# Optimization experiments

Measured on AMD Instinct MI355X. Metric: run time of the kernel, lower is better.

The kernel has to match this reference:

```python
import jax, jax.numpy as jnp
import numpy as np

TEMPERATURE = 0.08
NEG = -9e15  # matches torch masked_fill value
EPS = 1e-8   # F.cosine_similarity eps


def setup_inputs() -> dict:
    key = jax.random.key(0)
    inputs = jax.random.normal(key, (8192, 512), dtype=jnp.float32)
    return {"inputs": inputs}


def reference(inputs):
    N = inputs.shape[0]
    # cosine similarity via normalize + GEMM (avoids NxNxD broadcast)
    norms = jnp.maximum(jnp.linalg.norm(inputs, axis=-1, keepdims=True), EPS)
    z = inputs / norms
    sim = z @ z.T  # [N, N]
    # mask self-similarity BEFORE temperature scaling (as in the torch code)
    diag = jnp.eye(N, dtype=bool)
    sim = jnp.where(diag, NEG, sim)
    sim = sim / TEMPERATURE
    # positive of row i is column (i - N//2) % N (eye rolled by N//2 along dim 0)
    idx = jnp.arange(N)
    pos_idx = (idx - N // 2) % N
    pos = jnp.take_along_axis(sim, pos_idx[:, None], axis=1)[:, 0]  # [N]
    nll = jnp.mean(-pos + jax.scipy.special.logsumexp(sim, axis=-1))
    # rank of the positive: counting-based equivalent of
    # cat([pos, sim_masked]).argsort(desc).argmin() with stable ties
    masked = sim.at[idx, pos_idx].set(NEG)
    positive_ranking = jnp.sum(masked > pos[:, None], axis=-1)  # [N] int
    return positive_ranking, nll
```

## Files before the change

### kernel.cpp

```cpp
#include <hip/hip_runtime.h>
#include <cstdint>
#include <cstddef>

#define NROW 8192
#define DIM  512
#define HALF 4096
#define INV_T 12.5f
#define LDSW 64

typedef __bf16 bf16x8  __attribute__((ext_vector_type(8)));
typedef float  floatx4 __attribute__((ext_vector_type(4)));

__device__ __forceinline__ float bf2f_lo(unsigned u) { return __uint_as_float(u << 16); }
__device__ __forceinline__ float bf2f_hi(unsigned u) { return __uint_as_float(u & 0xffff0000u); }
__device__ __forceinline__ unsigned short f2bf(float f) {
    unsigned u = __float_as_uint(f);
    u += 0x7fffu + ((u >> 16) & 1u);
    return (unsigned short)(u >> 16);
}

__device__ __forceinline__ void atom_addf(float* p, float v) {
    __hip_atomic_fetch_add(p, v, __ATOMIC_RELAXED, __HIP_MEMORY_SCOPE_AGENT);
}

__global__ void knormpos(const float* __restrict__ x, unsigned short* __restrict__ z,
                         float* __restrict__ pos, float* __restrict__ sumexp,
                         float* __restrict__ cnt, float* __restrict__ nll_acc,
                         int* __restrict__ done) {
    int id = blockIdx.x * 256 + threadIdx.x;
    if (id < NROW) { sumexp[id] = 0.f; cnt[id] = 0.f; }
    if (id == 0) { nll_acc[0] = 0.f; done[0] = 0; }

    __shared__ __align__(16) unsigned short zs[4][512];

    const int w = threadIdx.x >> 6, lane = threadIdx.x & 63;
    const int row = blockIdx.x * 2 + (w & 1) + (w >> 1) * HALF;

    const float* xr = x + (size_t)row * DIM + lane * 8;
    float4 v0 = ((const float4*)xr)[0];
    float4 v1 = ((const float4*)xr)[1];
    float ss = v0.x*v0.x + v0.y*v0.y + v0.z*v0.z + v0.w*v0.w
             + v1.x*v1.x + v1.y*v1.y + v1.z*v1.z + v1.w*v1.w;
    #pragma unroll
    for (int m = 1; m < 64; m <<= 1) ss += __shfl_xor(ss, m);
    float inv = 1.0f / fmaxf(sqrtf(ss), 1e-8f);
    uint4 o;
    o.x = (unsigned)f2bf(v0.x * inv) | ((unsigned)f2bf(v0.y * inv) << 16);
    o.y = (unsigned)f2bf(v0.z * inv) | ((unsigned)f2bf(v0.w * inv) << 16);
    o.z = (unsigned)f2bf(v1.x * inv) | ((unsigned)f2bf(v1.y * inv) << 16);
    o.w = (unsigned)f2bf(v1.z * inv) | ((unsigned)f2bf(v1.w * inv) << 16);
    *(uint4*)(&zs[w][lane * 8]) = o;
    int sl = (lane & 56) | ((lane & 7) ^ (row & 7));
    *(uint4*)(z + (size_t)row * DIM + sl * 8) = o;
    __syncthreads();

    if (w < 2) {
        uint4 a = *(const uint4*)(&zs[w][lane * 8]);
        uint4 b = *(const uint4*)(&zs[w + 2][lane * 8]);
        float s = bf2f_lo(a.x)*bf2f_lo(b.x) + bf2f_hi(a.x)*bf2f_hi(b.x)
                + bf2f_lo(a.y)*bf2f_lo(b.y) + bf2f_hi(a.y)*bf2f_hi(b.y)
                + bf2f_lo(a.z)*bf2f_lo(b.z) + bf2f_hi(a.z)*bf2f_hi(b.z)
                + bf2f_lo(a.w)*bf2f_lo(b.w) + bf2f_hi(a.w)*bf2f_hi(b.w);
        #pragma unroll
        for (int m = 1; m < 64; m <<= 1) s += __shfl_xor(s, m);
        if (lane == 0) {
            const int r = blockIdx.x * 2 + w;
            pos[r] = s;
            pos[r + HALF] = s;
        }
    }
}

__global__ __launch_bounds__(512, 3) void kgemm(const unsigned short* __restrict__ z,
                                                const float* __restrict__ pos,
                                                float* __restrict__ sumexp,
                                                float* __restrict__ cnt) {
    __shared__ __align__(16) unsigned short As[128 * LDSW];
    __shared__ __align__(16) unsigned short Bs[128 * LDSW];
    __shared__ float pos_r[128];
    __shared__ float pos_c[128];

    const int b = blockIdx.x;
    int I = 0;
    while (b >= 516 * (I + 1) - 32 * (I + 1) * (I + 1)) ++I;
    const int lb = b - (516 * I - 32 * I * I);
    int bi, bj;
    if (lb < 36) {
        int ti = 0;
        while (lb >= 8 * (ti + 1) - (ti + 1) * ti / 2) ++ti;
        const int tj = ti + (lb - (8 * ti - ti * (ti - 1) / 2));
        bi = I * 8 + ti;
        bj = I * 8 + tj;
    } else {
        const int o = lb - 36;
        const int J = I + 1 + (o >> 6);
        bi = I * 8 + ((o & 63) >> 3);
        bj = J * 8 + (o & 7);
    }
    const int r0 = bi * 128;
    const int c0 = bj * 128;
    const bool offdiag = (bi != bj);

    const int t = threadIdx.x;
    const int w = t >> 6, lane = t & 63;
    const int wm = w >> 1, wn = w & 1;
    const int cid = lane & 15, q = lane >> 4;

    if (t < 128) pos_r[t] = pos[r0 + t];
    else if (t < 256) pos_c[t - 128] = pos[c0 + (t - 128)];

    floatx4 acc[2][4];
    #pragma unroll
    for (int i = 0; i < 2; ++i)
        #pragma unroll
        for (int j = 0; j < 4; ++j)
            acc[i][j] = floatx4{0.f, 0.f, 0.f, 0.f};

    const int lrow8 = lane >> 3;
    const int lcol  = (lane & 7) * 8;

    for (int kk = 0; kk < 8; ++kk) {
        const int k0 = kk * 64;
        #pragma unroll
        for (int it = 0; it < 2; ++it) {
            const int c = it * 8 + w;
            const unsigned short* gA = z + (size_t)(r0 + c * 8 + lrow8) * DIM + k0 + lcol;
            const unsigned short* gB = z + (size_t)(c0 + c * 8 + lrow8) * DIM + k0 + lcol;
            __builtin_amdgcn_global_load_lds(
                (const __attribute__((address_space(1))) unsigned int*)gA,
                (__attribute__((address_space(3))) unsigned int*)(As + c * 512),
                16, 0, 0);
            __builtin_amdgcn_global_load_lds(
                (const __attribute__((address_space(1))) unsigned int*)gB,
                (__attribute__((address_space(3))) unsigned int*)(Bs + c * 512),
                16, 0, 0);
        }
        __syncthreads();
        #pragma unroll
        for (int ks = 0; ks < 2; ++ks) {
            bf16x8 af[2], bfv[4];
            #pragma unroll
            for (int f = 0; f < 2; ++f) {
                const int ar = wm * 32 + f * 16 + cid;
                const int pa = (4 * ks + q) ^ (ar & 7);
                af[f] = *(const bf16x8*)(As + ar * LDSW + pa * 8);
            }
            #pragma unroll
            for (int f = 0; f < 4; ++f) {
                const int br = wn * 64 + f * 16 + cid;
                const int pb = (4 * ks + q) ^ (br & 7);
                bfv[f] = *(const bf16x8*)(Bs + br * LDSW + pb * 8);
            }
            #pragma unroll
            for (int fm = 0; fm < 2; ++fm)
                #pragma unroll
                for (int fn = 0; fn < 4; ++fn)
                    acc[fm][fn] = __builtin_amdgcn_mfma_f32_16x16x32_bf16(
                        af[fm], bfv[fn], acc[fm][fn], 0, 0, 0);
        }
        __syncthreads();
    }

    float col_e[4] = {0.f, 0.f, 0.f, 0.f};
    float col_c[4] = {0.f, 0.f, 0.f, 0.f};
    #pragma unroll
    for (int fm = 0; fm < 2; ++fm) {
        #pragma unroll
        for (int r = 0; r < 4; ++r) {
            const int li = wm * 32 + fm * 16 + q * 4 + r;
            const int i  = r0 + li;
            const float pv = pos_r[li];
            const int pj = (i + HALF) & (NROW - 1);
            float es = 0.f, cs = 0.f;
            #pragma unroll
            for (int fn = 0; fn < 4; ++fn) {
                const int lj = wn * 64 + fn * 16 + cid;
                const int j  = c0 + lj;
                const float s = acc[fm][fn][r];
                const float e = __expf((s - 1.0f) * INV_T);
                const bool dg = (j == i);
                es += dg ? 0.f : e;
                cs += (!dg && (j != pj) && (s > pv)) ? 1.f : 0.f;
                col_e[fn] += e;
                const int pjc = (j + HALF) & (NROW - 1);
                col_c[fn] += ((i != pjc) && (s > pos_c[lj])) ? 1.f : 0.f;
            }
            #pragma unroll
            for (int m = 1; m < 16; m <<= 1) {
                es += __shfl_xor(es, m);
                cs += __shfl_xor(cs, m);
            }
            if (cid == 0) {
                atom_addf(&sumexp[i], es);
                atom_addf(&cnt[i], cs);
            }
        }
    }

    if (offdiag) {
        #pragma unroll
        for (int fn = 0; fn < 4; ++fn) {
            float ec = col_e[fn], cc = col_c[fn];
            ec += __shfl_xor(ec, 16); ec += __shfl_xor(ec, 32);
            cc += __shfl_xor(cc, 16); cc += __shfl_xor(cc, 32);
            if (q == 0) {
                const int j = c0 + wn * 64 + fn * 16 + cid;
                atom_addf(&sumexp[j], ec);
                atom_addf(&cnt[j], cc);
            }
        }
    }
}

__global__ void NCELoss_3126736191777_kernel(const float* __restrict__ cnt,
                                             const float* __restrict__ sumexp,
                                             const float* __restrict__ pos,
                                             float* __restrict__ out,
                                             float* __restrict__ nll_acc,
                                             int* __restrict__ done) {
    __shared__ float red[4];
    const int t = threadIdx.x;
    const int r = blockIdx.x * 256 + t;
    float c = cnt[r], se = sumexp[r], p = pos[r];
    float v;
    if (p != p || fabsf(p) > 1.05f) v = 60000.0f;
    else if (se == 0.0f)            v = 40000.0f;
    else if (c < 0.0f)              v = 25000.0f;
    else                            v = c;
    out[r] = v;
    float local = -p * INV_T + INV_T + __logf(se);
    #pragma unroll
    for (int m = 1; m < 64; m <<= 1) local += __shfl_xor(local, m);
    if ((t & 63) == 0) red[t >> 6] = local;
    __syncthreads();
    if (t == 0) {
        atom_addf(nll_acc, red[0] + red[1] + red[2] + red[3]);
        __threadfence();
        int ticket = __hip_atomic_fetch_add(done, 1, __ATOMIC_ACQ_REL,
                                            __HIP_MEMORY_SCOPE_AGENT);
        if (ticket == (int)gridDim.x - 1) {
            __threadfence();
            out[NROW] = nll_acc[0] / (float)NROW;
        }
    }
}

extern "C" void kernel_launch(void* const* d_in, const int* in_sizes, int n_in,
                              void* d_out, int out_size, void* d_ws, size_t ws_size,
                              hipStream_t stream) {
    (void)in_sizes; (void)n_in; (void)out_size; (void)ws_size;
    const float* x = (const float*)d_in[0];

    char* base = (char*)d_ws;
    float* pos     = (float*)(base);
    float* sumexp  = (float*)(base + (size_t)NROW * 4);
    float* cnt     = (float*)(base + (size_t)NROW * 8);
    float* nll_acc = (float*)(base + (size_t)NROW * 12);
    int*   done    = (int*)(base + (size_t)NROW * 12 + 64);
    unsigned short* z = (unsigned short*)(base + (size_t)NROW * 12 + 4096);
    float* out = (float*)d_out;

    knormpos<<<NROW / 4, 256, 0, stream>>>(x, z, pos, sumexp, cnt, nll_acc, done);
    kgemm<<<2080, 512, 0, stream>>>(z, pos, sumexp, cnt);
    NCELoss_3126736191777_kernel<<<NROW / 256, 256, 0, stream>>>(cnt, sumexp, pos, out, nll_acc, done);
}
```

Before: 166.0 us.

## Enlarge GEMM block tile to 128x256 over symmetric upper-triangle tiles

```diff
diff --git a/kernel.cpp b/kernel.cpp
--- a/kernel.cpp
+++ b/kernel.cpp
@@ -76,42 +76,34 @@
                                                 float* __restrict__ sumexp,
                                                 float* __restrict__ cnt) {
     __shared__ __align__(16) unsigned short As[128 * LDSW];
-    __shared__ __align__(16) unsigned short Bs[128 * LDSW];
+    __shared__ __align__(16) unsigned short Bs[256 * LDSW];
     __shared__ float pos_r[128];
-    __shared__ float pos_c[128];
-
-    const int b = blockIdx.x;
-    int I = 0;
-    while (b >= 516 * (I + 1) - 32 * (I + 1) * (I + 1)) ++I;
-    const int lb = b - (516 * I - 32 * I * I);
-    int bi, bj;
-    if (lb < 36) {
-        int ti = 0;
-        while (lb >= 8 * (ti + 1) - (ti + 1) * ti / 2) ++ti;
-        const int tj = ti + (lb - (8 * ti - ti * (ti - 1) / 2));
-        bi = I * 8 + ti;
-        bj = I * 8 + tj;
-    } else {
-        const int o = lb - 36;
-        const int J = I + 1 + (o >> 6);
-        bi = I * 8 + ((o & 63) >> 3);
-        bj = J * 8 + (o & 7);
-    }
+    __shared__ float pos_c[256];
+
+    int rem = blockIdx.x;
+    int bi = 0;
+    while (rem >= 32 - (bi >> 1)) { rem -= 32 - (bi >> 1); ++bi; }
+    const int J = (bi >> 1) + rem;
+    const bool hasB0 = (2 * J >= bi);
     const int r0 = bi * 128;
-    const int c0 = bj * 128;
-    const bool offdiag = (bi != bj);
+    const int c00 = J * 256;
 
     const int t = threadIdx.x;
     const int w = t >> 6, lane = t & 63;
-    const int wm = w >> 1, wn = w & 1;
+    const int wm = w >> 2, wn = w & 3;
     const int cid = lane & 15, q = lane >> 4;
 
+    const int Tl = wn >> 1;
+    const int bjw = 2 * J + Tl;
+    const bool valid = (Tl == 1) || hasB0;
+    const bool offd  = (bjw != bi);
+
     if (t < 128) pos_r[t] = pos[r0 + t];
-    else if (t < 256) pos_c[t - 128] = pos[c0 + (t - 128)];
-
-    floatx4 acc[2][4];
-    #pragma unroll
-    for (int i = 0; i < 2; ++i)
+    else if (t < 384) pos_c[t - 128] = pos[c00 + (t - 128)];
+
+    floatx4 acc[4][4];
+    #pragma unroll
+    for (int i = 0; i < 4; ++i)
         #pragma unroll
         for (int j = 0; j < 4; ++j)
             acc[i][j] = floatx4{0.f, 0.f, 0.f, 0.f};
@@ -125,11 +117,15 @@
         for (int it = 0; it < 2; ++it) {
             const int c = it * 8 + w;
             const unsigned short* gA = z + (size_t)(r0 + c * 8 + lrow8) * DIM + k0 + lcol;
-            const unsigned short* gB = z + (size_t)(c0 + c * 8 + lrow8) * DIM + k0 + lcol;
             __builtin_amdgcn_global_load_lds(
                 (const __attribute__((address_space(1))) unsigned int*)gA,
                 (__attribute__((address_space(3))) unsigned int*)(As + c * 512),
                 16, 0, 0);
+        }
+        #pragma unroll
+        for (int it = 0; it < 4; ++it) {
+            const int c = it * 8 + w;
+            const unsigned short* gB = z + (size_t)(c00 + c * 8 + lrow8) * DIM + k0 + lcol;
             __builtin_amdgcn_global_load_lds(
                 (const __attribute__((address_space(1))) unsigned int*)gB,
                 (__attribute__((address_space(3))) unsigned int*)(Bs + c * 512),
@@ -138,21 +134,20 @@
         __syncthreads();
         #pragma unroll
         for (int ks = 0; ks < 2; ++ks) {
-            bf16x8 af[2], bfv[4];
-            #pragma unroll
-            for (int f = 0; f < 2; ++f) {
-                const int ar = wm * 32 + f * 16 + cid;
-                const int pa = (4 * ks + q) ^ (ar & 7);
-                af[f] = *(const bf16x8*)(As + ar * LDSW + pa * 8);
+            const int pkey = 4 * ks + q;
+            bf16x8 af[4], bfv[4];
+            #pragma unroll
+            for (int f = 0; f < 4; ++f) {
+                const int ar = wm * 64 + f * 16 + cid;
+                af[f] = *(const bf16x8*)(As + ar * LDSW + (pkey ^ (ar & 7)) * 8);
             }
             #pragma unroll
             for (int f = 0; f < 4; ++f) {
                 const int br = wn * 64 + f * 16 + cid;
-                const int pb = (4 * ks + q) ^ (br & 7);
-                bfv[f] = *(const bf16x8*)(Bs + br * LDSW + pb * 8);
-            }
-            #pragma unroll
-            for (int fm = 0; fm < 2; ++fm)
+                bfv[f] = *(const bf16x8*)(Bs + br * LDSW + (pkey ^ (br & 7)) * 8);
+            }
+            #pragma unroll
+            for (int fm = 0; fm < 4; ++fm)
                 #pragma unroll
                 for (int fn = 0; fn < 4; ++fn)
                     acc[fm][fn] = __builtin_amdgcn_mfma_f32_16x16x32_bf16(
@@ -161,13 +156,15 @@
         __syncthreads();
     }
 
+    if (!valid) return;
+
     float col_e[4] = {0.f, 0.f, 0.f, 0.f};
     float col_c[4] = {0.f, 0.f, 0.f, 0.f};
     #pragma unroll
-    for (int fm = 0; fm < 2; ++fm) {
+    for (int fm = 0; fm < 4; ++fm) {
         #pragma unroll
         for (int r = 0; r < 4; ++r) {
-            const int li = wm * 32 + fm * 16 + q * 4 + r;
+            const int li = wm * 64 + fm * 16 + q * 4 + r;
             const int i  = r0 + li;
             const float pv = pos_r[li];
             const int pj = (i + HALF) & (NROW - 1);
@@ -175,7 +172,7 @@
             #pragma unroll
             for (int fn = 0; fn < 4; ++fn) {
                 const int lj = wn * 64 + fn * 16 + cid;
-                const int j  = c0 + lj;
+                const int j  = c00 + lj;
                 const float s = acc[fm][fn][r];
                 const float e = __expf((s - 1.0f) * INV_T);
                 const bool dg = (j == i);
@@ -197,14 +194,14 @@
         }
     }
 
-    if (offdiag) {
+    if (offd) {
         #pragma unroll
         for (int fn = 0; fn < 4; ++fn) {
             float ec = col_e[fn], cc = col_c[fn];
             ec += __shfl_xor(ec, 16); ec += __shfl_xor(ec, 32);
             cc += __shfl_xor(cc, 16); cc += __shfl_xor(cc, 32);
             if (q == 0) {
-                const int j = c0 + wn * 64 + fn * 16 + cid;
+                const int j = c00 + wn * 64 + fn * 16 + cid;
                 atom_addf(&sumexp[j], ec);
                 atom_addf(&cnt[j], cc);
             }
@@ -261,6 +258,6 @@
     float* out = (float*)d_out;
 
     knormpos<<<NROW / 4, 256, 0, stream>>>(x, z, pos, sumexp, cnt, nll_acc, done);
-    kgemm<<<2080, 512, 0, stream>>>(z, pos, sumexp, cnt);
+    kgemm<<<1056, 512, 0, stream>>>(z, pos, sumexp, cnt);
     NCELoss_3126736191777_kernel<<<NROW / 256, 256, 0, stream>>>(cnt, sumexp, pos, out, nll_acc, done);
 }
```

New measurement: 192.7 us. 16.1% more time.
